# Kernel optimization log

Hardware: AMD Instinct MI355X
Metric: run time of the kernel (lower is better)

The kernel has to match this reference:

```python
import jax, jax.numpy as jnp
import numpy as np

B, S, D, DFF, E, TOP_K = 4, 2048, 1024, 4096, 8, 2


def setup_inputs() -> dict:
    key = jax.random.key(0)
    ks = jax.random.split(key, 6)
    s = 0.02
    return {
        "x": jax.random.normal(ks[0], (B, S, D), dtype=jnp.float32),
        "gate_w": jax.random.normal(ks[1], (E, D), dtype=jnp.float32) * s,
        "w1": jax.random.normal(ks[2], (E, DFF, D), dtype=jnp.float32) * s,
        "b1": jax.random.normal(ks[3], (E, DFF), dtype=jnp.float32) * s,
        "w2": jax.random.normal(ks[4], (E, D, DFF), dtype=jnp.float32) * s,
        "b2": jax.random.normal(ks[5], (E, D), dtype=jnp.float32) * s,
    }


def _moe_forward(x, gate_w, w1, b1, w2, b2):
    b, s, d = x.shape
    xf = x.reshape(-1, d)                      # [T, D]
    T = xf.shape[0]
    e = gate_w.shape[0]
    logits = xf @ gate_w.T                     # [T, E]
    top_v, top_i = jax.lax.top_k(logits, TOP_K)  # [T, K]
    gw = jax.nn.softmax(top_v, axis=-1)          # [T, K]
    # load-balance loss (Switch Transformers): E * sum_i f_i * P_i
    probs = jax.nn.softmax(logits, axis=-1)
    f = jnp.mean(jax.nn.one_hot(jnp.argmax(logits, axis=-1), e, dtype=x.dtype), axis=0)
    lb_loss = e * jnp.sum(f * probs.mean(axis=0))
    # dense per-expert FFN (exact GELU, matching torch F.gelu default)
    h = jax.nn.gelu(jnp.einsum('td,efd->tef', xf, w1) + b1, approximate=False)  # [T,E,DFF]
    eo = jnp.einsum('tef,edf->ted', h, w2) + b2                                  # [T,E,D]
    # scatter top-k gate weights into dense [T, E] combine weights
    cw = jnp.zeros((T, e), dtype=x.dtype).at[jnp.arange(T)[:, None], top_i].add(gw)
    out = jnp.einsum('te,ted->td', cw, eo).reshape(b, s, d)
    return out, lb_loss


def reference(x, gate_w, w1, b1, w2, b2):
    return _moe_forward(x, gate_w, w1, b1, w2, b2)
```

## Files before the change

kernel.cpp:

```cpp
#include <hip/hip_runtime.h>
#include <cstdint>
#include <cstddef>

#define NEXP 8
#define NTOK 8192
#define DMODEL 1024
#define DFFN 4096
#define CAP 17408

typedef __bf16 bf16;
typedef bf16 bf16x8 __attribute__((ext_vector_type(8)));
typedef float f32x4 __attribute__((ext_vector_type(4)));

static constexpr size_t OFF_HDR  = 0;
static constexpr size_t OFF_CNTH = 4096;
static constexpr size_t OFF_AMH  = OFF_CNTH + 65536;
static constexpr size_t OFF_PSH  = OFF_AMH + 65536;
static constexpr size_t OFF_TOKE = OFF_PSH + 65536;
static constexpr size_t OFF_TOKG = OFF_TOKE + 65536;
static constexpr size_t OFF_TOKS = OFF_TOKG + 65536;
static constexpr size_t OFF_BB   = OFF_TOKS + 65536;
static constexpr size_t OFF_XG   = OFF_BB + 65536;
static constexpr size_t OFF_W1B  = OFF_XG  + (size_t)CAP * DMODEL * 2;
static constexpr size_t OFF_W2B  = OFF_W1B + (size_t)NEXP * DFFN * DMODEL * 2;
static constexpr size_t OFF_H    = OFF_W2B + (size_t)NEXP * DMODEL * DFFN * 2;
static constexpr size_t OFF_O    = OFF_H   + (size_t)CAP * DFFN * 2;


__global__ void k_cvt(const float* __restrict__ s, bf16* __restrict__ d, int n8) {
    int i = blockIdx.x * 256 + threadIdx.x;
    if (i >= n8) return;
    const float4* sp = (const float4*)s;
    float4 a = sp[2 * i], b = sp[2 * i + 1];
    bf16x8 pk;
    pk[0] = (bf16)a.x; pk[1] = (bf16)a.y; pk[2] = (bf16)a.z; pk[3] = (bf16)a.w;
    pk[4] = (bf16)b.x; pk[5] = (bf16)b.y; pk[6] = (bf16)b.z; pk[7] = (bf16)b.w;
    ((bf16x8*)d)[i] = pk;
}

__global__ void k_gate(const float* __restrict__ x, const float* __restrict__ gwt,
                       int* __restrict__ cnth, int* __restrict__ amh, float* __restrict__ psh,
                       int* __restrict__ toke, float* __restrict__ tokg) {
    int tid = threadIdx.x, w = tid >> 6, lane = tid & 63;
    int t = blockIdx.x * 4 + w;
    __shared__ int s_cnt[8]; __shared__ int s_am[8]; __shared__ float s_ps[8];
    if (tid < 8) { s_cnt[tid] = 0; s_am[tid] = 0; s_ps[tid] = 0.f; }
    __syncthreads();
    float acc[8] = {0.f,0.f,0.f,0.f,0.f,0.f,0.f,0.f};
    const float4* xr = (const float4*)(x + (size_t)t * DMODEL);
#pragma unroll
    for (int c = 0; c < 4; c++) {
        float4 xv = xr[c * 64 + lane];
#pragma unroll
        for (int e = 0; e < 8; e++) {
            float4 wv = ((const float4*)(gwt + e * DMODEL))[c * 64 + lane];
            acc[e] = fmaf(xv.x, wv.x, fmaf(xv.y, wv.y, fmaf(xv.z, wv.z, fmaf(xv.w, wv.w, acc[e]))));
        }
    }
#pragma unroll
    for (int o = 32; o; o >>= 1) {
#pragma unroll
        for (int e = 0; e < 8; e++) acc[e] += __shfl_xor(acc[e], o);
    }
    if (lane == 0) {
        int i0 = 0; float v0 = acc[0];
#pragma unroll
        for (int e = 1; e < 8; e++) if (acc[e] > v0) { v0 = acc[e]; i0 = e; }
        int i1 = -1; float v1 = -1e30f;
#pragma unroll
        for (int e = 0; e < 8; e++) if (e != i0 && acc[e] > v1) { v1 = acc[e]; i1 = e; }
        float ex = expf(v1 - v0);
        float g0 = 1.f / (1.f + ex);
        float g1 = ex / (1.f + ex);
        toke[2 * t] = i0; toke[2 * t + 1] = i1;
        tokg[2 * t] = g0; tokg[2 * t + 1] = g1;
        atomicAdd(&s_cnt[i0], 1); atomicAdd(&s_cnt[i1], 1); atomicAdd(&s_am[i0], 1);
        float p[8], sum = 0.f;
#pragma unroll
        for (int e = 0; e < 8; e++) { p[e] = expf(acc[e] - v0); sum += p[e]; }
        float inv = 1.f / sum;
#pragma unroll
        for (int e = 0; e < 8; e++) atomicAdd(&s_ps[e], p[e] * inv);
    }
    __syncthreads();
    if (tid < 8) {
        cnth[blockIdx.x * 8 + tid] = s_cnt[tid];
        amh[blockIdx.x * 8 + tid]  = s_am[tid];
        psh[blockIdx.x * 8 + tid]  = s_ps[tid];
    }
}

__global__ void k_offsets(const int* __restrict__ cnth, const int* __restrict__ amh,
                          const float* __restrict__ psh, int* __restrict__ hdr,
                          int* __restrict__ bb, float* __restrict__ lb_out) {
    __shared__ int sc[8][256];
    __shared__ int sa[8][256];
    __shared__ float sp[8][256];
    __shared__ int sOff[8];
    int tid = threadIdx.x;
    int tc[8] = {0,0,0,0,0,0,0,0}, la[8] = {0,0,0,0,0,0,0,0};
    float lp[8] = {0.f,0.f,0.f,0.f,0.f,0.f,0.f,0.f};
    for (int j = 0; j < 8; j++) {
        int b = tid * 8 + j;
#pragma unroll
        for (int e = 0; e < 8; e++) { tc[e] += cnth[b * 8 + e]; la[e] += amh[b * 8 + e]; lp[e] += psh[b * 8 + e]; }
    }
#pragma unroll
    for (int e = 0; e < 8; e++) { sc[e][tid] = tc[e]; sa[e][tid] = la[e]; sp[e][tid] = lp[e]; }
    __syncthreads();
    for (int s = 1; s < 256; s <<= 1) {
        int add[8];
#pragma unroll
        for (int e = 0; e < 8; e++) add[e] = (tid >= s) ? sc[e][tid - s] : 0;
        __syncthreads();
#pragma unroll
        for (int e = 0; e < 8; e++) sc[e][tid] += add[e];
        __syncthreads();
    }
    for (int s = 128; s > 0; s >>= 1) {
        if (tid < s) {
#pragma unroll
            for (int e = 0; e < 8; e++) { sa[e][tid] += sa[e][tid + s]; sp[e][tid] += sp[e][tid + s]; }
        }
        __syncthreads();
    }
    if (tid == 0) {
        int run = 0; float lb = 0.f;
        for (int e = 0; e < 8; e++) {
            int c = sc[e][255];
            hdr[e] = c;
            hdr[16 + e] = run;
            int pad = ((c + 127) >> 7) << 7;
            hdr[24 + e] = pad;
            sOff[e] = run;
            run += pad;
            lb += ((float)sa[e][0] / (float)NTOK) * (sp[e][0] / (float)NTOK);
        }
        lb_out[0] = 8.f * lb;
    }
    __syncthreads();
    int excl[8];
#pragma unroll
    for (int e = 0; e < 8; e++) excl[e] = sOff[e] + sc[e][tid] - tc[e];
    for (int j = 0; j < 8; j++) {
        int b = tid * 8 + j;
#pragma unroll
        for (int e = 0; e < 8; e++) {
            bb[b * 8 + e] = excl[e];
            excl[e] += cnth[b * 8 + e];
        }
    }
}

__global__ void k_scatter(const float* __restrict__ x, const int* __restrict__ bb,
                          const int* __restrict__ toke, int* __restrict__ toks,
                          bf16* __restrict__ Xg) {
    int tid = threadIdx.x, w = tid >> 6, lane = tid & 63;
    int t = blockIdx.x * 4 + w;
    int a_e = (lane < 8) ? toke[blockIdx.x * 8 + lane] : 0;
    int e0 = __shfl(a_e, 2 * w), e1 = __shfl(a_e, 2 * w + 1);
    int r0 = 0, r1 = 0;
    for (int j = 0; j < 2 * w; j++) {
        int ej = __shfl(a_e, j);
        r0 += (ej == e0);
        r1 += (ej == e1);
    }
    int s0 = bb[blockIdx.x * 8 + e0] + r0;
    int s1 = bb[blockIdx.x * 8 + e1] + r1;
    if (lane == 0) { toks[2 * t] = s0; toks[2 * t + 1] = s1; }
    const float4* xr = (const float4*)(x + (size_t)t * DMODEL);
    bf16* d0 = Xg + (size_t)s0 * DMODEL;
    bf16* d1 = Xg + (size_t)s1 * DMODEL;
#pragma unroll
    for (int c = 0; c < 2; c++) {
        int base = c * 512 + lane * 8;
        float4 u = xr[base >> 2], v = xr[(base >> 2) + 1];
        bf16x8 pk;
        pk[0] = (bf16)u.x; pk[1] = (bf16)u.y; pk[2] = (bf16)u.z; pk[3] = (bf16)u.w;
        pk[4] = (bf16)v.x; pk[5] = (bf16)v.y; pk[6] = (bf16)v.z; pk[7] = (bf16)v.w;
        *(bf16x8*)(d0 + base) = pk;
        *(bf16x8*)(d1 + base) = pk;
    }
}

__global__ void k_zeropad(const int* __restrict__ hdr, bf16* __restrict__ Xg) {
    int e = blockIdx.x;
    int cnt = hdr[e], off = hdr[16 + e], padded = hdr[24 + e];
    int total = (padded - cnt) * (DMODEL / 8);
    bf16x8* base = (bf16x8*)(Xg + (size_t)(off + cnt) * DMODEL);
    bf16x8 z = {};
    for (int i = threadIdx.x; i < total; i += 256) base[i] = z;
}

__device__ __forceinline__ void gll16(const bf16* g, bf16* l) {
    __builtin_amdgcn_global_load_lds((const __attribute__((address_space(1))) unsigned int*)g,
                                     (__attribute__((address_space(3))) unsigned int*)l, 16, 0, 0);
}

__device__ __forceinline__ void wg_bar() {
    asm volatile("" ::: "memory");
    __builtin_amdgcn_s_barrier();
    asm volatile("" ::: "memory");
}

__device__ __forceinline__ float gelu_fast(float x) {
    float x3 = x * x * x;
    float z = fmaf(0.0713548163f, x3, 1.5957691216f * x);
    float s = __builtin_amdgcn_rcpf(1.0f + __expf(-z));
    return x * s;
}

template <int KD, int ND, bool GELU_BF16>
__global__ __launch_bounds__(512, 2) void k_gemm256(
    const bf16* __restrict__ Abase, const bf16* __restrict__ Wbase,
    const float* __restrict__ bias, void* __restrict__ Cbase,
    const int* __restrict__ hdr) {
    constexpr int NT = KD / 32;
    constexpr int GX = ND / 256;
    constexpr int GYX = GX * 32;
    extern __shared__ char smem[];

    int flat = blockIdx.x + GX * (blockIdx.y + 32 * blockIdx.z);
    constexpr int NPER = GYX * 8 / 8;
    int swz = (flat & 7) * NPER + (flat >> 3);
    int e   = swz / GYX;
    int rem = swz - e * GYX;
    int mt  = rem / GX;
    int nt  = rem - mt * GX;

    int padded = hdr[24 + e];
    if (mt * 256 >= padded) return;
    int mrem = padded - mt * 256; if (mrem > 256) mrem = 256;
    int row0 = hdr[16 + e] + mt * 256;

    const bf16* A = Abase + (size_t)row0 * KD;
    const bf16* W = Wbase + (size_t)e * ND * KD + (size_t)(nt * 256) * KD;

    int tid = threadIdx.x, wid = tid >> 6, lane = tid & 63;
    int srow   = (wid << 4) + (lane >> 2);
    int schunk = (lane & 3) ^ ((lane >> 2) & 3);
    int wr = wid & 1, wc = wid >> 1;
    int wm = wr << 7, wn = wc << 6;
    int fr = lane & 15, quad = lane >> 4;
    int rchoff = (quad ^ (fr & 3)) << 4;

    auto STAGE = [&](int u, int s) {
        int b = u & 3;
        int grow  = (s << 7) + srow;
        int garow = (grow < mrem) ? grow : 0;
        const bf16* ga = A + (size_t)garow * KD + u * 32 + (schunk << 3);
        const bf16* gb = W + (size_t)grow  * KD + u * 32 + (schunk << 3);
        bf16* la = (bf16*)(smem)         + (size_t)b * 8192 + (size_t)(((s << 7) + (wid << 4)) * 32);
        bf16* lb = (bf16*)(smem + 65536) + (size_t)b * 8192 + (size_t)(((s << 7) + (wid << 4)) * 32);
        gll16(ga, la);
        gll16(gb, lb);
    };
    auto LDA = [&](int t, int i) -> bf16x8 {
        const char* base = smem + (t & 3) * 16384;
        return *(const bf16x8*)(base + ((wm + i * 16 + fr) << 6) + rchoff);
    };
    auto LDB = [&](int t, int j) -> bf16x8 {
        const char* base = smem + 65536 + (t & 3) * 16384;
        return *(const bf16x8*)(base + ((wn + j * 16 + fr) << 6) + rchoff);
    };

    STAGE(0, 0); STAGE(0, 1); STAGE(1, 0); STAGE(1, 1);
    asm volatile("s_waitcnt vmcnt(4)" ::: "memory");
    wg_bar();

    f32x4 acc[8][4] = {};
    bf16x8 a4[4], b4[4];

#pragma unroll 1
    for (int t = 0; t < NT; ++t) {
#pragma unroll
        for (int j = 0; j < 4; j++) b4[j] = LDB(t, j);
#pragma unroll
        for (int i = 0; i < 4; i++) a4[i] = LDA(t, i);
        if (t + 2 < NT) STAGE(t + 2, 0);
        wg_bar();
        __builtin_amdgcn_s_setprio(1);
#pragma unroll
        for (int i = 0; i < 4; i++)
#pragma unroll
            for (int j = 0; j < 4; j++)
                acc[i][j] = __builtin_amdgcn_mfma_f32_16x16x32_bf16(a4[i], b4[j], acc[i][j], 0, 0, 0);
        __builtin_amdgcn_s_setprio(0);
        wg_bar();
#pragma unroll
        for (int i = 0; i < 4; i++) a4[i] = LDA(t, i + 4);
        if (t + 2 < NT) STAGE(t + 2, 1);
        wg_bar();
        __builtin_amdgcn_s_setprio(1);
#pragma unroll
        for (int i = 0; i < 4; i++)
#pragma unroll
            for (int j = 0; j < 4; j++)
                acc[i + 4][j] = __builtin_amdgcn_mfma_f32_16x16x32_bf16(a4[i], b4[j], acc[i + 4][j], 0, 0, 0);
        __builtin_amdgcn_s_setprio(0);
        if (t < NT - 2)      { asm volatile("s_waitcnt vmcnt(4)" ::: "memory"); }
        else if (t < NT - 1) { asm volatile("s_waitcnt vmcnt(0)" ::: "memory"); }
        wg_bar();
    }

#pragma unroll
    for (int j = 0; j < 4; j++) {
        int col = nt * 256 + wn + j * 16 + fr;
        float bv = bias[e * ND + col];
#pragma unroll
        for (int i = 0; i < 8; i++) {
#pragma unroll
            for (int r = 0; r < 4; r++) {
                int rowt = wm + i * 16 + quad * 4 + r;
                if (rowt < mrem) {
                    float v = acc[i][j][r] + bv;
                    size_t idx = (size_t)(row0 + rowt) * ND + col;
                    if (GELU_BF16) {
                        ((bf16*)Cbase)[idx] = (bf16)gelu_fast(v);
                    } else {
                        ((float*)Cbase)[idx] = v;
                    }
                }
            }
        }
    }
}

__global__ void k_combine(const float* __restrict__ O, const int* __restrict__ toks,
                          const float* __restrict__ tokg, float* __restrict__ out) {
    int t = blockIdx.x;
    int s0 = toks[2 * t], s1 = toks[2 * t + 1];
    float g0 = tokg[2 * t], g1 = tokg[2 * t + 1];
    const float4* o0 = (const float4*)(O + (size_t)s0 * DMODEL);
    const float4* o1 = (const float4*)(O + (size_t)s1 * DMODEL);
    float4* dst = (float4*)(out + (size_t)t * DMODEL);
    int i = threadIdx.x;
    float4 a = o0[i], b = o1[i];
    float4 r;
    r.x = g0 * a.x + g1 * b.x;
    r.y = g0 * a.y + g1 * b.y;
    r.z = g0 * a.z + g1 * b.z;
    r.w = g0 * a.w + g1 * b.w;
    dst[i] = r;
}

extern "C" void kernel_launch(void* const* d_in, const int* in_sizes, int n_in,
                              void* d_out, int out_size, void* d_ws, size_t ws_size,
                              hipStream_t stream) {
    const float* x   = (const float*)d_in[0];
    const float* gwt = (const float*)d_in[1];
    const float* w1  = (const float*)d_in[2];
    const float* b1  = (const float*)d_in[3];
    const float* w2  = (const float*)d_in[4];
    const float* b2  = (const float*)d_in[5];
    float* out = (float*)d_out;

    char* ws = (char*)d_ws;
    int*   hdr  = (int*)(ws + OFF_HDR);
    int*   cnth = (int*)(ws + OFF_CNTH);
    int*   amh  = (int*)(ws + OFF_AMH);
    float* psh  = (float*)(ws + OFF_PSH);
    int*   toke = (int*)(ws + OFF_TOKE);
    float* tokg = (float*)(ws + OFF_TOKG);
    int*   toks = (int*)(ws + OFF_TOKS);
    int*   bb   = (int*)(ws + OFF_BB);
    bf16*  Xg   = (bf16*)(ws + OFF_XG);
    bf16*  w1b  = (bf16*)(ws + OFF_W1B);
    bf16*  w2b  = (bf16*)(ws + OFF_W2B);
    bf16*  H    = (bf16*)(ws + OFF_H);
    float* O    = (float*)(ws + OFF_O);

    static bool s_attr = false;
    if (!s_attr) {
        (void)hipFuncSetAttribute(reinterpret_cast<const void*>(k_gemm256<DMODEL, DFFN, true>),
                                  hipFuncAttributeMaxDynamicSharedMemorySize, 131072);
        (void)hipFuncSetAttribute(reinterpret_cast<const void*>(k_gemm256<DFFN, DMODEL, false>),
                                  hipFuncAttributeMaxDynamicSharedMemorySize, 131072);
        s_attr = true;
    }

    k_cvt<<<16384, 256, 0, stream>>>(w1, w1b, 4194304);
    k_cvt<<<16384, 256, 0, stream>>>(w2, w2b, 4194304);
    k_gate<<<2048, 256, 0, stream>>>(x, gwt, cnth, amh, psh, toke, tokg);
    k_offsets<<<1, 256, 0, stream>>>(cnth, amh, psh, hdr, bb, out + (size_t)NTOK * DMODEL);
    k_zeropad<<<NEXP, 256, 0, stream>>>(hdr, Xg);
    k_scatter<<<2048, 256, 0, stream>>>(x, bb, toke, toks, Xg);
    dim3 g1(DFFN / 256, 32, NEXP);
    k_gemm256<DMODEL, DFFN, true><<<g1, 512, 131072, stream>>>(Xg, w1b, b1, (void*)H, hdr);
    dim3 g2(DMODEL / 256, 32, NEXP);
    k_gemm256<DFFN, DMODEL, false><<<g2, 512, 131072, stream>>>(H, w2b, b2, (void*)O, hdr);
    k_combine<<<NTOK, 256, 0, stream>>>(O, toks, tokg, out);
}
```

Before: 899.7 us.

## Retile expert GEMMs to 256x128 tiles with K64 steps and triple-buffered LDS

Changes the grouped GEMM tile from 256x256 with K=32 and a 4-slot ring to 256x128 with K=64 and a 3-slot ring. The LDS layout gets a 128-byte row stride with an XOR swizzle, and staging is split into halves. The block-to-expert mapping becomes a simple interleave (e = flat & 7). The grid doubles in the N dimension to give more blocks and halve the per-iteration barrier count. The cost is lower operand reuse per block and a larger LDS footprint (144KB).

```diff
diff --git a/kernel.cpp b/kernel.cpp
--- a/kernel.cpp
+++ b/kernel.cpp
@@ -215,16 +215,13 @@
     const bf16* __restrict__ Abase, const bf16* __restrict__ Wbase,
     const float* __restrict__ bias, void* __restrict__ Cbase,
     const int* __restrict__ hdr) {
-    constexpr int NT = KD / 32;
-    constexpr int GX = ND / 256;
-    constexpr int GYX = GX * 32;
+    constexpr int NT = KD / 64;
+    constexpr int GX = ND / 128;
     extern __shared__ char smem[];
 
     int flat = blockIdx.x + GX * (blockIdx.y + 32 * blockIdx.z);
-    constexpr int NPER = GYX * 8 / 8;
-    int swz = (flat & 7) * NPER + (flat >> 3);
-    int e   = swz / GYX;
-    int rem = swz - e * GYX;
+    int e   = flat & 7;
+    int rem = flat >> 3;
     int mt  = rem / GX;
     int nt  = rem - mt * GX;
 
@@ -234,78 +231,87 @@
     int row0 = hdr[16 + e] + mt * 256;
 
     const bf16* A = Abase + (size_t)row0 * KD;
-    const bf16* W = Wbase + (size_t)e * ND * KD + (size_t)(nt * 256) * KD;
+    const bf16* W = Wbase + (size_t)e * ND * KD + (size_t)(nt * 128) * KD;
 
     int tid = threadIdx.x, wid = tid >> 6, lane = tid & 63;
-    int srow   = (wid << 4) + (lane >> 2);
-    int schunk = (lane & 3) ^ ((lane >> 2) & 3);
-    int wr = wid & 1, wc = wid >> 1;
-    int wm = wr << 7, wn = wc << 6;
+    int srow8  = lane >> 3;
+    int schunk = (lane & 7) ^ srow8;
+    int wm = (wid & 1) << 7, wn = (wid >> 1) << 5;
     int fr = lane & 15, quad = lane >> 4;
-    int rchoff = (quad ^ (fr & 3)) << 4;
-
-    auto STAGE = [&](int u, int s) {
-        int b = u & 3;
-        int grow  = (s << 7) + srow;
-        int garow = (grow < mrem) ? grow : 0;
-        const bf16* ga = A + (size_t)garow * KD + u * 32 + (schunk << 3);
-        const bf16* gb = W + (size_t)grow  * KD + u * 32 + (schunk << 3);
-        bf16* la = (bf16*)(smem)         + (size_t)b * 8192 + (size_t)(((s << 7) + (wid << 4)) * 32);
-        bf16* lb = (bf16*)(smem + 65536) + (size_t)b * 8192 + (size_t)(((s << 7) + (wid << 4)) * 32);
-        gll16(ga, la);
-        gll16(gb, lb);
+    int swzr = quad ^ (fr & 7);
+
+    bf16* As = (bf16*)smem;
+    bf16* Bs = (bf16*)(smem + 98304);
+
+    auto STAGE_H = [&](int u, int sl, int h) {
+        int a0 = (h * 2) * 64 + wid * 8;
+        int a1 = a0 + 64;
+        int b0 = h * 64 + wid * 8;
+        int gra = a0 + srow8; if (gra >= mrem) gra = 0;
+        int grb = a1 + srow8; if (grb >= mrem) grb = 0;
+        gll16(A + (size_t)gra * KD + u * 64 + schunk * 8, As + sl * 16384 + a0 * 64);
+        gll16(A + (size_t)grb * KD + u * 64 + schunk * 8, As + sl * 16384 + a1 * 64);
+        gll16(W + (size_t)(b0 + srow8) * KD + u * 64 + schunk * 8, Bs + sl * 8192 + b0 * 64);
     };
-    auto LDA = [&](int t, int i) -> bf16x8 {
-        const char* base = smem + (t & 3) * 16384;
-        return *(const bf16x8*)(base + ((wm + i * 16 + fr) << 6) + rchoff);
+    auto LDA = [&](int sl, int i, int kx) -> bf16x8 {
+        return *(const bf16x8*)((const char*)As + sl * 32768 +
+                                ((wm + i * 16 + fr) << 7) + ((swzr ^ (kx << 2)) << 4));
     };
-    auto LDB = [&](int t, int j) -> bf16x8 {
-        const char* base = smem + 65536 + (t & 3) * 16384;
-        return *(const bf16x8*)(base + ((wn + j * 16 + fr) << 6) + rchoff);
+    auto LDB = [&](int sl, int j, int kx) -> bf16x8 {
+        return *(const bf16x8*)((const char*)Bs + sl * 16384 +
+                                ((wn + j * 16 + fr) << 7) + ((swzr ^ (kx << 2)) << 4));
     };
 
-    STAGE(0, 0); STAGE(0, 1); STAGE(1, 0); STAGE(1, 1);
-    asm volatile("s_waitcnt vmcnt(4)" ::: "memory");
+    STAGE_H(0, 0, 0); STAGE_H(0, 0, 1);
+    STAGE_H(1, 1, 0); STAGE_H(1, 1, 1);
+    asm volatile("s_waitcnt vmcnt(6)" ::: "memory");
     wg_bar();
 
-    f32x4 acc[8][4] = {};
-    bf16x8 a4[4], b4[4];
+    f32x4 acc[8][2] = {};
+    int sl = 0;
 
 #pragma unroll 1
     for (int t = 0; t < NT; ++t) {
-#pragma unroll
-        for (int j = 0; j < 4; j++) b4[j] = LDB(t, j);
-#pragma unroll
-        for (int i = 0; i < 4; i++) a4[i] = LDA(t, i);
-        if (t + 2 < NT) STAGE(t + 2, 0);
+        int sl2 = sl + 2; if (sl2 >= 3) sl2 -= 3;
+        bf16x8 a4[4][2], b4[2][2];
+#pragma unroll
+        for (int j = 0; j < 2; j++) { b4[j][0] = LDB(sl, j, 0); b4[j][1] = LDB(sl, j, 1); }
+#pragma unroll
+        for (int i = 0; i < 4; i++) { a4[i][0] = LDA(sl, i, 0); a4[i][1] = LDA(sl, i, 1); }
+        if (t + 2 < NT) STAGE_H(t + 2, sl2, 0);
         wg_bar();
         __builtin_amdgcn_s_setprio(1);
 #pragma unroll
         for (int i = 0; i < 4; i++)
 #pragma unroll
-            for (int j = 0; j < 4; j++)
-                acc[i][j] = __builtin_amdgcn_mfma_f32_16x16x32_bf16(a4[i], b4[j], acc[i][j], 0, 0, 0);
+            for (int j = 0; j < 2; j++) {
+                acc[i][j] = __builtin_amdgcn_mfma_f32_16x16x32_bf16(a4[i][0], b4[j][0], acc[i][j], 0, 0, 0);
+                acc[i][j] = __builtin_amdgcn_mfma_f32_16x16x32_bf16(a4[i][1], b4[j][1], acc[i][j], 0, 0, 0);
+            }
         __builtin_amdgcn_s_setprio(0);
         wg_bar();
 #pragma unroll
-        for (int i = 0; i < 4; i++) a4[i] = LDA(t, i + 4);
-        if (t + 2 < NT) STAGE(t + 2, 1);
+        for (int i = 0; i < 4; i++) { a4[i][0] = LDA(sl, i + 4, 0); a4[i][1] = LDA(sl, i + 4, 1); }
+        if (t + 2 < NT) STAGE_H(t + 2, sl2, 1);
         wg_bar();
         __builtin_amdgcn_s_setprio(1);
 #pragma unroll
         for (int i = 0; i < 4; i++)
 #pragma unroll
-            for (int j = 0; j < 4; j++)
-                acc[i + 4][j] = __builtin_amdgcn_mfma_f32_16x16x32_bf16(a4[i], b4[j], acc[i + 4][j], 0, 0, 0);
+            for (int j = 0; j < 2; j++) {
+                acc[i + 4][j] = __builtin_amdgcn_mfma_f32_16x16x32_bf16(a4[i][0], b4[j][0], acc[i + 4][j], 0, 0, 0);
+                acc[i + 4][j] = __builtin_amdgcn_mfma_f32_16x16x32_bf16(a4[i][1], b4[j][1], acc[i + 4][j], 0, 0, 0);
+            }
         __builtin_amdgcn_s_setprio(0);
-        if (t < NT - 2)      { asm volatile("s_waitcnt vmcnt(4)" ::: "memory"); }
-        else if (t < NT - 1) { asm volatile("s_waitcnt vmcnt(0)" ::: "memory"); }
+        if (t + 2 < NT)      { asm volatile("s_waitcnt vmcnt(6)" ::: "memory"); }
+        else if (t + 1 < NT) { asm volatile("s_waitcnt vmcnt(0)" ::: "memory"); }
         wg_bar();
-    }
-
-#pragma unroll
-    for (int j = 0; j < 4; j++) {
-        int col = nt * 256 + wn + j * 16 + fr;
+        sl = sl + 1; if (sl == 3) sl = 0;
+    }
+
+#pragma unroll
+    for (int j = 0; j < 2; j++) {
+        int col = nt * 128 + wn + j * 16 + fr;
         float bv = bias[e * ND + col];
 #pragma unroll
         for (int i = 0; i < 8; i++) {
@@ -373,9 +379,9 @@
     static bool s_attr = false;
     if (!s_attr) {
         (void)hipFuncSetAttribute(reinterpret_cast<const void*>(k_gemm256<DMODEL, DFFN, true>),
-                                  hipFuncAttributeMaxDynamicSharedMemorySize, 131072);
+                                  hipFuncAttributeMaxDynamicSharedMemorySize, 147456);
         (void)hipFuncSetAttribute(reinterpret_cast<const void*>(k_gemm256<DFFN, DMODEL, false>),
-                                  hipFuncAttributeMaxDynamicSharedMemorySize, 131072);
+                                  hipFuncAttributeMaxDynamicSharedMemorySize, 147456);
         s_attr = true;
     }
 
@@ -385,9 +391,9 @@
     k_offsets<<<1, 256, 0, stream>>>(cnth, amh, psh, hdr, bb, out + (size_t)NTOK * DMODEL);
     k_zeropad<<<NEXP, 256, 0, stream>>>(hdr, Xg);
     k_scatter<<<2048, 256, 0, stream>>>(x, bb, toke, toks, Xg);
-    dim3 g1(DFFN / 256, 32, NEXP);
-    k_gemm256<DMODEL, DFFN, true><<<g1, 512, 131072, stream>>>(Xg, w1b, b1, (void*)H, hdr);
-    dim3 g2(DMODEL / 256, 32, NEXP);
-    k_gemm256<DFFN, DMODEL, false><<<g2, 512, 131072, stream>>>(H, w2b, b2, (void*)O, hdr);
+    dim3 g1(DFFN / 128, 32, NEXP);
+    k_gemm256<DMODEL, DFFN, true><<<g1, 512, 147456, stream>>>(Xg, w1b, b1, (void*)H, hdr);
+    dim3 g2(DMODEL / 128, 32, NEXP);
+    k_gemm256<DFFN, DMODEL, false><<<g2, 512, 147456, stream>>>(H, w2b, b2, (void*)O, hdr);
     k_combine<<<NTOK, 256, 0, stream>>>(O, toks, tokg, out);
 }
```

Measured after the change: 853.0 us. 5.2% less time.
